# Kernel tuning notes

Measured on AMD Instinct MI355X. Metric: run time of the kernel, lower is better.

Reference implementation:

```python
import jax, jax.numpy as jnp
import numpy as np

SINKHORN_ITERS = 5
EPS = 1e-12  # torch F.normalize eps


def _l2norm(x):
    n = jnp.sqrt(jnp.sum(x * x, axis=-1, keepdims=True))
    return x / jnp.maximum(n, EPS)


def setup_inputs() -> dict:
    key = jax.random.key(0)
    k1, k2, k3, k4 = jax.random.split(key, 4)
    B, Nd, Ns, D, Dm = 8, 2048, 2048, 1024, 256
    drone_nodes = jax.random.normal(k1, (B, Nd, D), dtype=jnp.float32)
    sat_nodes = jax.random.normal(k2, (B, Ns, D), dtype=jnp.float32)
    # match_proj parameters (nn.Linear(d_model, match_dim))
    lim = 1.0 / np.sqrt(D)
    W = jax.random.uniform(k3, (D, Dm), minval=-lim, maxval=lim, dtype=jnp.float32)
    b = jax.random.uniform(k4, (Dm,), minval=-lim, maxval=lim, dtype=jnp.float32)
    return {"drone_nodes": drone_nodes, "sat_nodes": sat_nodes, "W": W, "b": b}


def reference(drone_nodes, sat_nodes, W, b):
    # project + L2-normalize each node embedding
    d = _l2norm(drone_nodes @ W + b)   # [B, Nd, Dm]
    s = _l2norm(sat_nodes @ W + b)     # [B, Ns, Dm]
    M0 = jnp.einsum('bnd,bmd->bnm', d, s)  # [B, Nd, Ns] cosine similarities
    M = M0
    for _ in range(SINKHORN_ITERS):
        M = M - jax.nn.logsumexp(M, axis=2, keepdims=True)
        M = M - jax.nn.logsumexp(M, axis=1, keepdims=True)
    assignment = jnp.exp(M)
    denom = min(d.shape[1], s.shape[1])
    match_score = jnp.sum(assignment * M0, axis=(1, 2)) / denom  # [B]
    return (assignment, match_score)
```

## Files before the change

kernel.cpp:

```cpp
#include <hip/hip_runtime.h>
#include <math.h>

#define BATCH 8
#define NNODE 2048
#define DIN   1024
#define DM    256
#define ROWS_TOTAL (BATCH * NNODE)

#define Q127  0.011359803471566641f
#define INV127 0.007874015748031496f

typedef unsigned short u16;
typedef __attribute__((ext_vector_type(8))) short short8;
typedef __attribute__((ext_vector_type(4))) float f32x4;

__device__ __forceinline__ u16 f2b(float f) {
    union { float f; unsigned u; } v; v.f = f;
    unsigned r = v.u + 0x7fffu + ((v.u >> 16) & 1u);
    return (u16)(r >> 16);
}
__device__ __forceinline__ float dqi(unsigned wd, int k) {
    return (float)((int)(wd << ((3 - k) * 8)) >> 24);
}

__global__ __launch_bounds__(256) void cvgm_prep_w(
    const float* __restrict__ W, u16* __restrict__ Wt)
{
    __shared__ float t[32][33];
    const int tx = threadIdx.x & 31, ty = threadIdx.x >> 5;
    const int k0 = blockIdx.x * 32, c0 = blockIdx.y * 32;
    #pragma unroll
    for (int r = 0; r < 4; ++r) {
        const int kl = ty * 4 + r;
        t[kl][tx] = W[(size_t)(k0 + kl) * DM + c0 + tx];
    }
    __syncthreads();
    #pragma unroll
    for (int r = 0; r < 4; ++r) {
        const int cl = ty * 4 + r;
        Wt[(size_t)(c0 + cl) * DIN + k0 + tx] = f2b(t[tx][cl]);
    }
}

__global__ __launch_bounds__(512) void cvgm_proj_mfma(
    const float* __restrict__ Xd, const float* __restrict__ Xs,
    const u16* __restrict__ Wt, const float* __restrict__ bias,
    u16* __restrict__ Pd, u16* __restrict__ Ps)
{
    __shared__ u16 As[64 * 64];
    __shared__ u16 Bs[256 * 64];
    __shared__ float rsum[4][64];

    const float* X = blockIdx.y ? Xs : Xd;
    u16* P = blockIdx.y ? Ps : Pd;

    const int tid = threadIdx.x;
    const int lane = tid & 63, wid = tid >> 6;
    const int wr = wid >> 2, wc = wid & 3;
    const int l15 = lane & 15, l4 = lane >> 4;
    const int row0 = blockIdx.x * 64;

    f32x4 acc[2][4];
    #pragma unroll
    for (int m = 0; m < 2; ++m)
        #pragma unroll
        for (int n = 0; n < 4; ++n) acc[m][n] = (f32x4){0.f, 0.f, 0.f, 0.f};

    const int arow = tid >> 3, ac = tid & 7;

    for (int k0 = 0; k0 < DIN; k0 += 64) {
        const float* src = X + (size_t)(row0 + arow) * DIN + k0 + ac * 8;
        const float4 x0 = *(const float4*)src;
        const float4 x1 = *(const float4*)(src + 4);
        short8 wb[4];
        #pragma unroll
        for (int it = 0; it < 4; ++it) {
            const int id = it * 512 + tid;
            const int col = id >> 3, cc = id & 7;
            wb[it] = *(const short8*)(Wt + (size_t)col * DIN + k0 + cc * 8);
        }
        __syncthreads();
        short8 ap;
        ap[0]=(short)f2b(x0.x); ap[1]=(short)f2b(x0.y); ap[2]=(short)f2b(x0.z); ap[3]=(short)f2b(x0.w);
        ap[4]=(short)f2b(x1.x); ap[5]=(short)f2b(x1.y); ap[6]=(short)f2b(x1.z); ap[7]=(short)f2b(x1.w);
        *(short8*)(As + (arow * 8 + (ac ^ (arow & 7))) * 8) = ap;
        #pragma unroll
        for (int it = 0; it < 4; ++it) {
            const int id = it * 512 + tid;
            const int col = id >> 3, cc = id & 7;
            *(short8*)(Bs + (col * 8 + (cc ^ (col & 7))) * 8) = wb[it];
        }
        __syncthreads();
        #pragma unroll
        for (int ks = 0; ks < 2; ++ks) {
            const int ch = ks * 4 + l4;
            short8 af[2], bfr[4];
            #pragma unroll
            for (int m = 0; m < 2; ++m) {
                const int row = wr * 32 + m * 16 + l15;
                af[m] = *(const short8*)(As + (row * 8 + (ch ^ (row & 7))) * 8);
            }
            #pragma unroll
            for (int n = 0; n < 4; ++n) {
                const int col = wc * 64 + n * 16 + l15;
                bfr[n] = *(const short8*)(Bs + (col * 8 + (ch ^ (col & 7))) * 8);
            }
            #pragma unroll
            for (int m = 0; m < 2; ++m)
                #pragma unroll
                for (int n = 0; n < 4; ++n)
                    acc[m][n] = __builtin_amdgcn_mfma_f32_16x16x32_bf16(af[m], bfr[n], acc[m][n], 0, 0, 0);
        }
        __syncthreads();
    }

    #pragma unroll
    for (int n = 0; n < 4; ++n) {
        const float bv = bias[wc * 64 + n * 16 + l15];
        #pragma unroll
        for (int m = 0; m < 2; ++m)
            #pragma unroll
            for (int r = 0; r < 4; ++r) acc[m][n][r] += bv;
    }
    #pragma unroll
    for (int m = 0; m < 2; ++m)
        #pragma unroll
        for (int r = 0; r < 4; ++r) {
            float s = 0.f;
            #pragma unroll
            for (int n = 0; n < 4; ++n) s += acc[m][n][r] * acc[m][n][r];
            s += __shfl_xor(s, 1); s += __shfl_xor(s, 2);
            s += __shfl_xor(s, 4); s += __shfl_xor(s, 8);
            if (l15 == 0) rsum[wc][wr * 32 + m * 16 + l4 * 4 + r] = s;
        }
    __syncthreads();
    #pragma unroll
    for (int m = 0; m < 2; ++m)
        #pragma unroll
        for (int r = 0; r < 4; ++r) {
            const int row = wr * 32 + m * 16 + l4 * 4 + r;
            const float tot = rsum[0][row] + rsum[1][row] + rsum[2][row] + rsum[3][row];
            const float inv = 1.0f / fmaxf(sqrtf(tot), 1e-12f);
            #pragma unroll
            for (int n = 0; n < 4; ++n) {
                const int col = wc * 64 + n * 16 + l15;
                P[(size_t)(row0 + row) * DM + col] = f2b(acc[m][n][r] * inv);
            }
        }
}

__global__ __launch_bounds__(256) void cvgm_m0_mfma(
    const u16* __restrict__ Dp, const u16* __restrict__ Sp,
    char* __restrict__ Cq)
{
    __shared__ u16 As[128 * 64];
    __shared__ u16 Bs[128 * 64];

    const int tid = threadIdx.x;
    const int lane = tid & 63, wid = tid >> 6;
    const int wr = wid >> 1, wc = wid & 1;
    const int l15 = lane & 15, l4 = lane >> 4;
    const int bb = blockIdx.z;
    const int i0 = blockIdx.y * 128, j0 = blockIdx.x * 128;
    const u16* Db = Dp + (size_t)bb * NNODE * DM;
    const u16* Sb = Sp + (size_t)bb * NNODE * DM;

    f32x4 acc[4][4];
    #pragma unroll
    for (int m = 0; m < 4; ++m)
        #pragma unroll
        for (int n = 0; n < 4; ++n) acc[m][n] = (f32x4){0.f, 0.f, 0.f, 0.f};

    for (int k0 = 0; k0 < DM; k0 += 64) {
        short8 ra[4], rb[4];
        #pragma unroll
        for (int it = 0; it < 4; ++it) {
            const int id = it * 256 + tid;
            const int row = id >> 3, c = id & 7;
            ra[it] = *(const short8*)(Db + (size_t)(i0 + row) * DM + k0 + c * 8);
            rb[it] = *(const short8*)(Sb + (size_t)(j0 + row) * DM + k0 + c * 8);
        }
        __syncthreads();
        #pragma unroll
        for (int it = 0; it < 4; ++it) {
            const int id = it * 256 + tid;
            const int row = id >> 3, c = id & 7;
            const int sl = row * 8 + (c ^ (row & 7));
            *(short8*)(As + sl * 8) = ra[it];
            *(short8*)(Bs + sl * 8) = rb[it];
        }
        __syncthreads();
        #pragma unroll
        for (int ks = 0; ks < 2; ++ks) {
            const int ch = ks * 4 + l4;
            short8 af[4], bfr[4];
            #pragma unroll
            for (int m = 0; m < 4; ++m) {
                const int row = wr * 64 + m * 16 + l15;
                af[m] = *(const short8*)(As + (row * 8 + (ch ^ (row & 7))) * 8);
            }
            #pragma unroll
            for (int n = 0; n < 4; ++n) {
                const int col = wc * 64 + n * 16 + l15;
                bfr[n] = *(const short8*)(Bs + (col * 8 + (ch ^ (col & 7))) * 8);
            }
            #pragma unroll
            for (int m = 0; m < 4; ++m)
                #pragma unroll
                for (int n = 0; n < 4; ++n)
                    acc[m][n] = __builtin_amdgcn_mfma_f32_16x16x32_bf16(af[m], bfr[n], acc[m][n], 0, 0, 0);
        }
        __syncthreads();
    }

    char* Cqb = Cq + (size_t)bb * NNODE * NNODE;
    #pragma unroll
    for (int m = 0; m < 4; ++m) {
        const int row = i0 + wr * 64 + m * 16 + l4 * 4;
        #pragma unroll
        for (int n = 0; n < 4; ++n) {
            const int col = j0 + wc * 64 + n * 16 + l15;
            #pragma unroll
            for (int r = 0; r < 4; ++r) {
                int q = __float2int_rn(acc[m][n][r] * 127.f);
                q = q > 127 ? 127 : (q < -127 ? -127 : q);
                Cqb[(size_t)(row + r) * NNODE + col] = (char)q;
            }
        }
    }
}

template <int FIRST>
__global__ __launch_bounds__(256) void cvgm_rc(
    const char* __restrict__ Mq, const float* __restrict__ Sin,
    float* __restrict__ euo, float* __restrict__ ps)
{
    __shared__ float cps[4][NNODE];

    const int tid = threadIdx.x;
    const int lane = tid & 63, w = tid >> 6;
    const int b = blockIdx.y, chunk = blockIdx.x;
    const size_t row0 = ((size_t)b << 11) + chunk * 16;
    const char* gb = Mq + row0 * NNODE + lane * 16;

    float wv[32];
    if constexpr (FIRST) {
        #pragma unroll
        for (int k = 0; k < 32; ++k) wv[k] = 1.f;
    } else {
        const float* Sb = Sin + (b << 11);
        #pragma unroll
        for (int s = 0; s < 2; ++s)
            #pragma unroll
            for (int k = 0; k < 4; ++k) {
                const float4 vv = *(const float4*)(Sb + s * 1024 + lane * 16 + k * 4);
                wv[s*16+k*4+0] = 1.0f / vv.x;
                wv[s*16+k*4+1] = 1.0f / vv.y;
                wv[s*16+k*4+2] = 1.0f / vv.z;
                wv[s*16+k*4+3] = 1.0f / vv.w;
            }
    }

    float sc[32];
    #pragma unroll
    for (int k = 0; k < 32; ++k) sc[k] = 0.f;

    #pragma unroll
    for (int rr = 0; rr < 4; ++rr) {
        const char* rsrc = gb + (size_t)(w * 4 + rr) * NNODE;
        const int4 d0 = *(const int4*)(rsrc);
        const int4 d1 = *(const int4*)(rsrc + 1024);
        const unsigned qd[8] = {(unsigned)d0.x, (unsigned)d0.y, (unsigned)d0.z, (unsigned)d0.w,
                                (unsigned)d1.x, (unsigned)d1.y, (unsigned)d1.z, (unsigned)d1.w};
        float p[32];
        #pragma unroll
        for (int q = 0; q < 8; ++q)
            #pragma unroll
            for (int k = 0; k < 4; ++k)
                p[q * 4 + k] = exp2f(dqi(qd[q], k) * Q127);
        float s = 0.f;
        #pragma unroll
        for (int k = 0; k < 32; ++k) s = fmaf(p[k], wv[k], s);
        #pragma unroll
        for (int off = 1; off < 64; off <<= 1) s += __shfl_xor(s, off);
        const float eu = 1.0f / s;
        if (lane == 0) euo[row0 + w * 4 + rr] = eu;
        #pragma unroll
        for (int k = 0; k < 32; ++k) sc[k] = fmaf(p[k], eu, sc[k]);
    }

    #pragma unroll
    for (int s = 0; s < 2; ++s)
        #pragma unroll
        for (int k = 0; k < 4; ++k)
            *(float4*)(&cps[w][s * 1024 + lane * 16 + k * 4]) =
                make_float4(sc[s*16+k*4+0], sc[s*16+k*4+1], sc[s*16+k*4+2], sc[s*16+k*4+3]);
    __syncthreads();

    const int j = tid * 8;
    float4 a0 = *(const float4*)(&cps[0][j]), a1 = *(const float4*)(&cps[0][j + 4]);
    #pragma unroll
    for (int ww = 1; ww < 4; ++ww) {
        const float4 b0 = *(const float4*)(&cps[ww][j]);
        const float4 b1 = *(const float4*)(&cps[ww][j + 4]);
        a0.x += b0.x; a0.y += b0.y; a0.z += b0.z; a0.w += b0.w;
        a1.x += b1.x; a1.y += b1.y; a1.z += b1.z; a1.w += b1.w;
    }
    float* dst = ps + ((size_t)(b * 128 + chunk)) * NNODE + j;
    *(float4*)dst = a0;
    *(float4*)(dst + 4) = a1;
}

__global__ __launch_bounds__(256) void cvgm_merge(
    const float* __restrict__ ps, float* __restrict__ colsum)
{
    const int idx = blockIdx.x * 256 + threadIdx.x;
    const int b = idx >> 11, j = idx & 2047;
    float s = 0.f;
    #pragma unroll 8
    for (int c = 0; c < 128; ++c) s += ps[(size_t)(b * 128 + c) * NNODE + j];
    colsum[idx] = s;
}

__global__ __launch_bounds__(256) void cvgm_final(
    const char* __restrict__ Mq, const float* __restrict__ eui,
    const float* __restrict__ Scol, float* __restrict__ out,
    float* __restrict__ spart)
{
    const int tid = threadIdx.x;
    const int lane = tid & 63, w = tid >> 6;
    const int b = blockIdx.y, chunk = blockIdx.x;
    const size_t row0 = ((size_t)b << 11) + chunk * 16;
    const char* gb = Mq + row0 * NNODE + lane * 16;

    float wv[32];
    {
        const float* Sb = Scol + (b << 11);
        #pragma unroll
        for (int s = 0; s < 2; ++s)
            #pragma unroll
            for (int k = 0; k < 4; ++k) {
                const float4 vv = *(const float4*)(Sb + s * 1024 + lane * 16 + k * 4);
                wv[s*16+k*4+0] = 1.0f / vv.x;
                wv[s*16+k*4+1] = 1.0f / vv.y;
                wv[s*16+k*4+2] = 1.0f / vv.z;
                wv[s*16+k*4+3] = 1.0f / vv.w;
            }
    }

    #pragma unroll
    for (int rr = 0; rr < 4; ++rr) {
        const size_t row = row0 + w * 4 + rr;
        const char* rsrc = gb + (size_t)(w * 4 + rr) * NNODE;
        float* drow = out + row * NNODE + lane * 16;
        const float eu = eui[row];
        const int4 d0 = *(const int4*)(rsrc);
        const int4 d1 = *(const int4*)(rsrc + 1024);
        const unsigned qd[8] = {(unsigned)d0.x, (unsigned)d0.y, (unsigned)d0.z, (unsigned)d0.w,
                                (unsigned)d1.x, (unsigned)d1.y, (unsigned)d1.z, (unsigned)d1.w};
        float acc = 0.f;
        #pragma unroll
        for (int q = 0; q < 8; ++q) {
            float e[4];
            #pragma unroll
            for (int k = 0; k < 4; ++k) {
                const float xq = dqi(qd[q], k);
                e[k] = exp2f(xq * Q127) * eu * wv[q * 4 + k];
                acc = fmaf(e[k], xq, acc);
            }
            *(float4*)(drow + (q >> 2) * 1024 + (q & 3) * 4) = make_float4(e[0], e[1], e[2], e[3]);
        }
        #pragma unroll
        for (int off = 1; off < 64; off <<= 1) acc += __shfl_xor(acc, off);
        if (lane == 0) spart[row] = acc * INV127;
    }
}

__global__ __launch_bounds__(256) void cvgm_score(
    const float* __restrict__ spart, float* __restrict__ score)
{
    const int b = blockIdx.x;
    float acc = 0.f;
    for (int t = threadIdx.x; t < NNODE; t += 256) acc += spart[(b << 11) + t];
    #pragma unroll
    for (int off = 1; off < 64; off <<= 1) acc += __shfl_xor(acc, off);
    __shared__ float sh[4];
    if ((threadIdx.x & 63) == 0) sh[threadIdx.x >> 6] = acc;
    __syncthreads();
    if (threadIdx.x == 0) score[b] = (sh[0] + sh[1] + sh[2] + sh[3]) * (1.0f / 2048.0f);
}

extern "C" void kernel_launch(void* const* d_in, const int* in_sizes, int n_in,
                              void* d_out, int out_size, void* d_ws, size_t ws_size,
                              hipStream_t stream) {
    (void)in_sizes; (void)n_in; (void)out_size; (void)ws_size;
    const float* drone = (const float*)d_in[0];
    const float* sat   = (const float*)d_in[1];
    const float* W     = (const float*)d_in[2];
    const float* bias  = (const float*)d_in[3];

    float* out   = (float*)d_out;
    float* score = out + (size_t)BATCH * NNODE * NNODE;

    char* ws = (char*)d_ws;
    const size_t SZ_M0Q  = (size_t)BATCH * NNODE * NNODE;
    const size_t SZ_PROJ = (size_t)ROWS_TOTAL * DM * 2;
    const size_t SZ_WT   = (size_t)DM * DIN * 2;
    const size_t SZ_UV   = (size_t)ROWS_TOTAL * 4;
    const size_t SZ_PS   = (size_t)BATCH * 128 * NNODE * 4;

    size_t off = 0;
    char* M0q  = ws + off;            off += SZ_M0Q;
    u16* dproj = (u16*)(ws + off);    off += SZ_PROJ;
    u16* sproj = (u16*)(ws + off);    off += SZ_PROJ;
    u16* Wt    = (u16*)(ws + off);    off += SZ_WT;
    float* colsum = (float*)(ws + off); off += SZ_UV;
    float* eu   = (float*)(ws + off); off += SZ_UV;
    float* ps   = (float*)(ws + off); off += SZ_PS;
    float* spart = (float*)(ws + off);

    cvgm_prep_w<<<dim3(32, 8), 256, 0, stream>>>(W, Wt);
    cvgm_proj_mfma<<<dim3(256, 2), 512, 0, stream>>>(drone, sat, Wt, bias, dproj, sproj);
    cvgm_m0_mfma<<<dim3(16, 16, 8), 256, 0, stream>>>(dproj, sproj, M0q);

    cvgm_rc<1><<<dim3(128, 8), 256, 0, stream>>>(M0q, colsum, eu, ps);
    cvgm_merge<<<ROWS_TOTAL / 256, 256, 0, stream>>>(ps, colsum);
    for (int it = 1; it < 5; ++it) {
        cvgm_rc<0><<<dim3(128, 8), 256, 0, stream>>>(M0q, colsum, eu, ps);
        cvgm_merge<<<ROWS_TOTAL / 256, 256, 0, stream>>>(ps, colsum);
    }

    cvgm_final<<<dim3(128, 8), 256, 0, stream>>>(M0q, eu, colsum, out, spart);
    cvgm_score<<<BATCH, 256, 0, stream>>>(spart, score);
}
```

Before: 261.3 us.

## Load GEMM tiles directly into LDS and stage int8 output for coalesced stores

Both the projection GEMM (W tile) and the similarity GEMM (D/S tiles) now use global_load_lds to copy 16-byte chunks straight into swizzled LDS, skipping the register round trip. The trailing barrier of each k-iteration is dropped. The int8 similarity output is first written into LDS and then stored to global memory as 16-byte rows instead of scattered single-byte stores. A possible risk is that removing the trailing barrier lets the next iteration's direct LDS loads overwrite tiles other waves are still reading, since the leading barrier may not order these asynchronous loads.

```diff
diff --git a/kernel.cpp b/kernel.cpp
--- a/kernel.cpp
+++ b/kernel.cpp
@@ -14,6 +14,10 @@
 typedef __attribute__((ext_vector_type(8))) short short8;
 typedef __attribute__((ext_vector_type(4))) float f32x4;
 
+#define GLD16(gp, lp) __builtin_amdgcn_global_load_lds( \
+    (const __attribute__((address_space(1))) void*)(gp), \
+    (__attribute__((address_space(3))) void*)(lp), 16, 0, 0)
+
 __device__ __forceinline__ u16 f2b(float f) {
     union { float f; unsigned u; } v; v.f = f;
     unsigned r = v.u + 0x7fffu + ((v.u >> 16) & 1u);
@@ -72,24 +76,19 @@
         const float* src = X + (size_t)(row0 + arow) * DIN + k0 + ac * 8;
         const float4 x0 = *(const float4*)src;
         const float4 x1 = *(const float4*)(src + 4);
-        short8 wb[4];
-        #pragma unroll
-        for (int it = 0; it < 4; ++it) {
-            const int id = it * 512 + tid;
-            const int col = id >> 3, cc = id & 7;
-            wb[it] = *(const short8*)(Wt + (size_t)col * DIN + k0 + cc * 8);
-        }
         __syncthreads();
+        #pragma unroll
+        for (int i = 0; i < 4; ++i) {
+            const int s = (wid * 4 + i) * 64 + lane;
+            const int col = s >> 3, sc = s & 7;
+            const int cc = sc ^ (col & 7);
+            GLD16(Wt + (size_t)col * DIN + k0 + cc * 8,
+                  Bs + (size_t)((wid * 4 + i) * 64) * 8);
+        }
         short8 ap;
         ap[0]=(short)f2b(x0.x); ap[1]=(short)f2b(x0.y); ap[2]=(short)f2b(x0.z); ap[3]=(short)f2b(x0.w);
         ap[4]=(short)f2b(x1.x); ap[5]=(short)f2b(x1.y); ap[6]=(short)f2b(x1.z); ap[7]=(short)f2b(x1.w);
         *(short8*)(As + (arow * 8 + (ac ^ (arow & 7))) * 8) = ap;
-        #pragma unroll
-        for (int it = 0; it < 4; ++it) {
-            const int id = it * 512 + tid;
-            const int col = id >> 3, cc = id & 7;
-            *(short8*)(Bs + (col * 8 + (cc ^ (col & 7))) * 8) = wb[it];
-        }
         __syncthreads();
         #pragma unroll
         for (int ks = 0; ks < 2; ++ks) {
@@ -111,7 +110,6 @@
                 for (int n = 0; n < 4; ++n)
                     acc[m][n] = __builtin_amdgcn_mfma_f32_16x16x32_bf16(af[m], bfr[n], acc[m][n], 0, 0, 0);
         }
-        __syncthreads();
     }
 
     #pragma unroll
@@ -172,22 +170,16 @@
         for (int n = 0; n < 4; ++n) acc[m][n] = (f32x4){0.f, 0.f, 0.f, 0.f};
 
     for (int k0 = 0; k0 < DM; k0 += 64) {
-        short8 ra[4], rb[4];
-        #pragma unroll
-        for (int it = 0; it < 4; ++it) {
-            const int id = it * 256 + tid;
-            const int row = id >> 3, c = id & 7;
-            ra[it] = *(const short8*)(Db + (size_t)(i0 + row) * DM + k0 + c * 8);
-            rb[it] = *(const short8*)(Sb + (size_t)(j0 + row) * DM + k0 + c * 8);
-        }
         __syncthreads();
         #pragma unroll
-        for (int it = 0; it < 4; ++it) {
-            const int id = it * 256 + tid;
-            const int row = id >> 3, c = id & 7;
-            const int sl = row * 8 + (c ^ (row & 7));
-            *(short8*)(As + sl * 8) = ra[it];
-            *(short8*)(Bs + sl * 8) = rb[it];
+        for (int i = 0; i < 4; ++i) {
+            const int s = (wid * 4 + i) * 64 + lane;
+            const int row = s >> 3, sc = s & 7;
+            const int cc = sc ^ (row & 7);
+            GLD16(Db + (size_t)(i0 + row) * DM + k0 + cc * 8,
+                  As + (size_t)((wid * 4 + i) * 64) * 8);
+            GLD16(Sb + (size_t)(j0 + row) * DM + k0 + cc * 8,
+                  Bs + (size_t)((wid * 4 + i) * 64) * 8);
         }
         __syncthreads();
         #pragma unroll
@@ -210,23 +202,31 @@
                 for (int n = 0; n < 4; ++n)
                     acc[m][n] = __builtin_amdgcn_mfma_f32_16x16x32_bf16(af[m], bfr[n], acc[m][n], 0, 0, 0);
         }
-        __syncthreads();
-    }
-
-    char* Cqb = Cq + (size_t)bb * NNODE * NNODE;
+    }
+
+    __syncthreads();
+    char* Cs = (char*)As;
     #pragma unroll
     for (int m = 0; m < 4; ++m) {
-        const int row = i0 + wr * 64 + m * 16 + l4 * 4;
+        const int rl = wr * 64 + m * 16 + l4 * 4;
         #pragma unroll
         for (int n = 0; n < 4; ++n) {
-            const int col = j0 + wc * 64 + n * 16 + l15;
+            const int cl = wc * 64 + n * 16 + l15;
             #pragma unroll
             for (int r = 0; r < 4; ++r) {
                 int q = __float2int_rn(acc[m][n][r] * 127.f);
                 q = q > 127 ? 127 : (q < -127 ? -127 : q);
-                Cqb[(size_t)(row + r) * NNODE + col] = (char)q;
-            }
-        }
+                Cs[(rl + r) * 128 + cl] = (char)q;
+            }
+        }
+    }
+    __syncthreads();
+    char* Cqb = Cq + (size_t)bb * NNODE * NNODE;
+    const int lrow = tid >> 1, lcol = (tid & 1) * 64;
+    #pragma unroll
+    for (int i = 0; i < 4; ++i) {
+        const int4 v = *(const int4*)(Cs + lrow * 128 + lcol + i * 16);
+        *(int4*)(Cqb + (size_t)(i0 + lrow) * NNODE + j0 + lcol + i * 16) = v;
     }
 }
 
```

After: 261.3 us. No clear change (-0.0%).
